# Optimization experiments

Hardware: AMD Instinct MI355X
Metric: run time of the kernel (lower is better)

The kernel has to match this reference:

```python
import jax, jax.numpy as jnp
import numpy as np

NUM_HEADS = 16


def setup_inputs() -> dict:
    key = jax.random.key(0)
    ks = jax.random.split(key, 6)
    B, S, H = 4, 2048, 1024
    x = jax.random.normal(ks[0], (B, S, H), dtype=jnp.float32)
    mask = jax.random.randint(ks[1], (B, 1, 1, S), 0, 2, dtype=jnp.int32)
    scale = 1.0 / np.sqrt(H)
    Wq = jax.random.normal(ks[2], (H, H), dtype=jnp.float32) * scale
    Wk = jax.random.normal(ks[3], (H, H), dtype=jnp.float32) * scale
    Wv = jax.random.normal(ks[4], (H, H), dtype=jnp.float32) * scale
    Wo = jax.random.normal(ks[5], (H, H), dtype=jnp.float32) * scale
    bo = jnp.zeros((H,), dtype=jnp.float32)
    return {"x": x, "mask": mask, "Wq": Wq, "Wk": Wk, "Wv": Wv, "Wo": Wo, "bo": bo}


def reference(x, mask, Wq, Wk, Wv, Wo, bo):
    B, S, H = x.shape
    nh = NUM_HEADS
    dk = H // nh

    def split_heads(t):  # (B,S,H) -> (B,nh,S,dk)
        return t.reshape(B, S, nh, dk).transpose(0, 2, 1, 3)

    # torch Linear: y = x @ W.T (q/k/v bias-free)
    q = split_heads(x @ Wq.T)
    k = split_heads(x @ Wk.T)
    v = split_heads(x @ Wv.T)

    scores = jnp.einsum('bhqd,bhkd->bhqk', q, k) / jnp.sqrt(jnp.float32(dk))
    scores = jnp.where(mask == 0, jnp.float32(-1e9), scores)
    attn = jax.nn.softmax(scores, axis=-1)  # dropout is identity in eval mode
    out = jnp.einsum('bhqk,bhkd->bhqd', attn, v)
    out = out.transpose(0, 2, 1, 3).reshape(B, S, H)
    return out @ Wo.T + bo
```

## Files before the change

### kernel.cpp

```cpp
#include <hip/hip_runtime.h>
#include <hip/hip_bf16.h>

typedef __attribute__((ext_vector_type(8))) short sh8;
typedef __attribute__((ext_vector_type(4))) float f32x4;

#define MFMA16(a, b, c) __builtin_amdgcn_mfma_f32_16x16x32_bf16((a), (b), (c), 0, 0, 0)

__device__ __forceinline__ unsigned short f2bf(float f) {
    return (unsigned short)((__float_as_uint(f) + 0x8000u) >> 16);
}
__device__ __forceinline__ unsigned int pack2bf(float lo, float hi) {
    unsigned int ul = __float_as_uint(lo) + 0x8000u;
    unsigned int uh = __float_as_uint(hi) + 0x8000u;
    return __builtin_amdgcn_perm(uh, ul, 0x07060302u);
}
__device__ __forceinline__ float redmax_hi(float x) {
    x = fmaxf(x, __shfl_xor(x, 16, 64));
    return fmaxf(x, __shfl_xor(x, 32, 64));
}
__device__ __forceinline__ float redsum_hi(float x) {
    x += __shfl_xor(x, 16, 64);
    return x + __shfl_xor(x, 32, 64);
}
__device__ __forceinline__ void gload_lds16(const void* g, void* l) {
    __builtin_amdgcn_global_load_lds(
        (const __attribute__((address_space(1))) unsigned int*)g,
        (__attribute__((address_space(3))) unsigned int*)l, 16, 0, 0);
}

__global__ __launch_bounds__(256) void cvt_x_k(
    const float* __restrict__ src, unsigned short* __restrict__ dst, int n4)
{
    int i = blockIdx.x * 256 + threadIdx.x;
    int stride = gridDim.x * 256;
    for (; i < n4; i += stride) {
        float4 v = ((const float4*)src)[i];
        uint2 h = { pack2bf(v.x, v.y), pack2bf(v.z, v.w) };
        ((uint2*)dst)[i] = h;
    }
}
__global__ __launch_bounds__(256) void cvt_w_k(
    const float* __restrict__ Wq, const float* __restrict__ Wk,
    const float* __restrict__ Wv, const float* __restrict__ Wo,
    unsigned short* __restrict__ wbf)
{
    int i = blockIdx.x * 256 + threadIdx.x;
    int seg = i >> 18;
    int off = i & 0x3FFFF;
    const float* s = (seg < 2) ? ((seg == 0) ? Wq : Wk) : ((seg == 2) ? Wv : Wo);
    float4 v = ((const float4*)s)[off];
    uint2 h = { pack2bf(v.x, v.y), pack2bf(v.z, v.w) };
    ((uint2*)wbf)[i] = h;
}

__global__ __launch_bounds__(64) void compact_k(
    const int* __restrict__ mask, int* __restrict__ idx, int* __restrict__ cnt)
{
    const int b = blockIdx.x, l = threadIdx.x;
    const int* mb = mask + b * 2048;
    int base = 0;
    for (int i = 0; i < 32; ++i) {
        int m = mb[i * 64 + l];
        unsigned long long bal = __ballot(m != 0);
        int pre = __popcll(bal & ((1ull << l) - 1ull));
        if (m) idx[b * 2048 + base + pre] = i * 64 + l;
        base += (int)__popcll(bal);
    }
    if (base == 0) {
        for (int i = l; i < 2048; i += 64) idx[b * 2048 + i] = i;
        base = 2048;
    }
    if (l == 0) cnt[b] = base;
}

__global__ __launch_bounds__(256) void kvgather_k(
    const unsigned short* __restrict__ qkv, const int* __restrict__ idx,
    const int* __restrict__ cnt, unsigned short* __restrict__ Kck, int b0)
{
    const int b = blockIdx.z;
    const int t = blockIdx.y;
    const int z = blockIdx.x;
    const int nc = cnt[b0 + b];
    if (t * 64 >= ((nc + 63) & ~63)) return;
    const int* idxb = idx + (size_t)(b0 + b) * 2048;
    const int tid = threadIdx.x;
    unsigned short* dst_b = Kck + (size_t)b * 2048 * 1024;
#pragma unroll
    for (int p = 0; p < 4; ++p) {
        int i = p * 256 + tid;
        int r = t * 64 + z * 8 + (i >> 7);
        int c = i & 127;
        int src = idxb[min(r, nc - 1)];
        uint4 v = *(const uint4*)&qkv[((size_t)b * 2048 + src) * 3072 + 1024 + c * 8];
        *(uint4*)&dst_b[(size_t)r * 1024 + c * 8] = v;
    }
}

__global__ __launch_bounds__(256) void vtrans_k(
    const unsigned short* __restrict__ qkv, const int* __restrict__ idx,
    const int* __restrict__ cnt, unsigned short* __restrict__ Vtg, int b0)
{
    __shared__ unsigned short Ls[128][72];
    const int kb = blockIdx.x;
    const int h  = blockIdx.y;
    const int b  = blockIdx.z;
    const int nc = cnt[b0 + b];
    if (kb * 128 >= ((nc + 63) & ~63)) return;
    const int* idxb = idx + (size_t)(b0 + b) * 2048;
    const int tid = threadIdx.x;
#pragma unroll
    for (int p = 0; p < 4; ++p) {
        int i = p * 256 + tid;
        int r = i >> 3, c = i & 7;
        int src = idxb[min(kb * 128 + r, nc - 1)];
        uint4 v = *(const uint4*)&qkv[((size_t)b * 2048 + src) * 3072 + 2048 + h * 64 + c * 8];
        *(uint4*)&Ls[r][c * 8] = v;
    }
    __syncthreads();
    unsigned short* dst = Vtg + ((size_t)b * 16 + h) * 64 * 2048;
#pragma unroll
    for (int p = 0; p < 4; ++p) {
        int i = p * 256 + tid;
        int d = i >> 4, kc = i & 15;
        unsigned int wv[4];
#pragma unroll
        for (int j = 0; j < 4; ++j) {
            unsigned int lo = Ls[kc * 8 + 2 * j][d];
            unsigned int hv = Ls[kc * 8 + 2 * j + 1][d];
            wv[j] = lo | (hv << 16);
        }
        *(uint4*)&dst[(size_t)d * 2048 + kb * 128 + kc * 8] = *(uint4*)wv;
    }
}

__global__ __launch_bounds__(256) void gemm_qkv_k(
    const unsigned short* __restrict__ xbf,
    const unsigned short* __restrict__ wbf,
    unsigned short* __restrict__ qkv)
{
    __shared__ unsigned short As[128][32];
    __shared__ unsigned short Bs[128][32];
    const int tid = threadIdx.x;
    const int l = tid & 63, w = tid >> 6;
    const int wr = w >> 1, wc = w & 1;
    const long row0 = (long)blockIdx.y * 128;
    const int col0 = blockIdx.x * 128;

    f32x4 acc[4][4] = {};
    const int fr = l & 15, hi = l >> 4;

    const int sr = tid >> 2;
    const int sc = (tid & 3) * 8;
    const unsigned short* ga = &xbf[(row0 + sr) * 1024 + sc];
    const unsigned short* gb = &wbf[(long)(col0 + sr) * 1024 + sc];
    unsigned short* la = &As[w * 16][0];
    unsigned short* lb = &Bs[w * 16][0];

    for (int k0 = 0; k0 < 1024; k0 += 32) {
        __syncthreads();
        gload_lds16(ga + k0, la);
        gload_lds16(ga + 64 * 1024 + k0, la + 64 * 32);
        gload_lds16(gb + k0, lb);
        gload_lds16(gb + 64 * 1024 + k0, lb + 64 * 32);
        __syncthreads();

        sh8 af[4], bf[4];
#pragma unroll
        for (int i = 0; i < 4; ++i) {
            af[i] = *(const sh8*)&As[wr * 64 + i * 16 + fr][hi * 8];
            bf[i] = *(const sh8*)&Bs[wc * 64 + i * 16 + fr][hi * 8];
        }
#pragma unroll
        for (int i = 0; i < 4; ++i)
#pragma unroll
            for (int j = 0; j < 4; ++j)
                acc[i][j] = MFMA16(af[i], bf[j], acc[i][j]);
    }

    const float scale = (col0 < 1024) ? 0.1803368801f : 1.0f;
    const int rg = hi * 4, cg = l & 15;
#pragma unroll
    for (int i = 0; i < 4; ++i)
#pragma unroll
        for (int j = 0; j < 4; ++j) {
            long gr = row0 + wr * 64 + i * 16 + rg;
            int gc = col0 + wc * 64 + j * 16 + cg;
#pragma unroll
            for (int r = 0; r < 4; ++r)
                qkv[(gr + r) * 3072 + gc] = f2bf(acc[i][j][r] * scale);
        }
}

__global__ __launch_bounds__(256) void attn_k(
    const unsigned short* __restrict__ qkv, const unsigned short* __restrict__ Kck,
    const unsigned short* __restrict__ Vtg, const int* __restrict__ cnt,
    unsigned short* __restrict__ ao, int b0)
{
    __shared__ unsigned short Kl[64][64];
    __shared__ unsigned short Vt[64][64];
    __shared__ float biasf[64];
    __shared__ unsigned short Pl[4][16][72];

    const int tid = threadIdx.x;
    const int l = tid & 63, w = tid >> 6;
    const int fr = l & 15, hi = l >> 4;

    int nwg = gridDim.x;
    int wgid = ((nwg & 7) == 0) ? ((blockIdx.x & 7) * (nwg >> 3) + (blockIdx.x >> 3))
                                : blockIdx.x;
    const int qb = wgid & 31;
    const int h  = (wgid >> 5) & 15;
    const int b  = wgid >> 9;
    const int q0 = qb * 64;
    const long base = (long)b * 2048;

    const int nc = cnt[b0 + b];
    const int nt = (nc + 63) >> 6;

    sh8 qf0, qf1;
    {
        const unsigned short* qp = &qkv[(base + q0 + w * 16 + fr) * 3072 + h * 64 + hi * 8];
        qf0 = *(const sh8*)qp;
        qf1 = *(const sh8*)(qp + 32);
    }

    f32x4 acc[4] = {};
    float mrow = -1e30f;
    float lrow = 0.f;

    const long TSK = 131072;
    const char* kck_b = (const char*)Kck + (size_t)b * 2048 * 2048;

    const int l8 = l >> 3, c8 = l & 7;
    const char* ksrc = kck_b + (size_t)(w * 16 + l8) * 2048 + h * 128 + ((c8 ^ l8) * 16);
    unsigned short* kdst0 = &Kl[w * 16][0];
    unsigned short* kdst1 = &Kl[w * 16 + 8][0];

    const char* vtg_h = (const char*)Vtg + ((size_t)b * 16 + h) * 64 * 4096;
    const int d0 = w * 16 + l8, d1 = d0 + 8;
    const int fd0 = (d0 & 7) ^ (d0 >> 3), fd1 = (d1 & 7) ^ (d1 >> 3);
    const char* vsrc0 = vtg_h + (size_t)d0 * 4096 + ((c8 ^ fd0) * 16);
    const char* vsrc1 = vtg_h + (size_t)d1 * 4096 + ((c8 ^ fd1) * 16);
    unsigned short* vdst0 = &Vt[w * 16][0];
    unsigned short* vdst1 = &Vt[w * 16 + 8][0];

    if (tid < 64) biasf[tid] = ((nt - 1) * 64 + tid < nc) ? 0.0f : -1e9f;

    for (int t = 0; t < nt; ++t) {
        __syncthreads();
        gload_lds16(ksrc, kdst0);
        gload_lds16(ksrc + 8 * 2048, kdst1);
        ksrc += TSK;
        gload_lds16(vsrc0, vdst0);
        gload_lds16(vsrc1, vdst1);
        vsrc0 += 128; vsrc1 += 128;
        __syncthreads();

        sh8 kf[4][2];
#pragma unroll
        for (int tt = 0; tt < 4; ++tt) {
            const unsigned short* kp = &Kl[tt * 16 + fr][0];
#pragma unroll
            for (int c = 0; c < 2; ++c)
                kf[tt][c] = *(const sh8*)&kp[((4 * c + hi) ^ (fr & 7)) * 8];
        }

        f32x4 s[4] = {};
        __builtin_amdgcn_s_setprio(1);
#pragma unroll
        for (int tt = 0; tt < 4; ++tt) {
            s[tt] = MFMA16(kf[tt][0], qf0, s[tt]);
            s[tt] = MFMA16(kf[tt][1], qf1, s[tt]);
        }
        __builtin_amdgcn_s_setprio(0);

        if (t == nt - 1) {
#pragma unroll
            for (int tt = 0; tt < 4; ++tt)
                s[tt] += *(const f32x4*)&biasf[tt * 16 + 4 * hi];
        }

        float pm = s[0][0];
#pragma unroll
        for (int tt = 0; tt < 4; ++tt)
#pragma unroll
            for (int r = 0; r < 4; ++r) pm = fmaxf(pm, s[tt][r]);
        pm = redmax_hi(pm);

        if (!__all(pm <= mrow)) {
            float mn = fmaxf(mrow, pm);
            float scl = __builtin_amdgcn_exp2f(mrow - mn);
            lrow *= scl;
#pragma unroll
            for (int df = 0; df < 4; ++df) acc[df] *= scl;
            mrow = mn;
        }

        float ps = 0.f;
#pragma unroll
        for (int tt = 0; tt < 4; ++tt)
#pragma unroll
            for (int r = 0; r < 4; ++r) {
                float p = __builtin_amdgcn_exp2f(s[tt][r] - mrow);
                s[tt][r] = p;
                ps += p;
            }
        lrow += redsum_hi(ps);

#pragma unroll
        for (int tt = 0; tt < 4; ++tt) {
            uint2 pw = { pack2bf(s[tt][0], s[tt][1]), pack2bf(s[tt][2], s[tt][3]) };
            *(uint2*)&Pl[w][fr][tt * 16 + hi * 4] = pw;
        }

#pragma unroll
        for (int c = 0; c < 2; ++c) {
            sh8 pa = *(const sh8*)&Pl[w][fr][c * 32 + hi * 8];
            __builtin_amdgcn_s_setprio(1);
#pragma unroll
            for (int df = 0; df < 4; ++df) {
                int d = df * 16 + fr;
                int fd = (d & 7) ^ (d >> 3);
                sh8 vfr = *(const sh8*)&Vt[d][((4 * c + hi) ^ fd) * 8];
                acc[df] = MFMA16(vfr, pa, acc[df]);
            }
            __builtin_amdgcn_s_setprio(0);
        }
    }

    {
        float inv = 1.0f / lrow;
        long qr = base + q0 + w * 16 + fr;
        unsigned short* op = &ao[qr * 1024 + h * 64];
#pragma unroll
        for (int df = 0; df < 4; ++df) {
            f32x4 o = acc[df];
            uint2 ow = { pack2bf(o[0] * inv, o[1] * inv), pack2bf(o[2] * inv, o[3] * inv) };
            *(uint2*)&op[df * 16 + hi * 4] = ow;
        }
    }
}

__global__ __launch_bounds__(256) void gemm_out_k(
    const unsigned short* __restrict__ ao, const unsigned short* __restrict__ wob,
    const float* __restrict__ bo, float* __restrict__ out)
{
    __shared__ unsigned short As[128][32];
    __shared__ unsigned short Bs[128][32];
    const int tid = threadIdx.x;
    const int l = tid & 63, w = tid >> 6;
    const int wr = w >> 1, wc = w & 1;
    const long row0 = (long)blockIdx.y * 128;
    const int col0 = blockIdx.x * 128;

    f32x4 acc[4][4] = {};
    const int fr = l & 15, hi = l >> 4;

    const int sr = tid >> 2;
    const int sc = (tid & 3) * 8;
    const unsigned short* ga = &ao[(row0 + sr) * 1024 + sc];
    const unsigned short* gb = &wob[(long)(col0 + sr) * 1024 + sc];
    unsigned short* la = &As[w * 16][0];
    unsigned short* lb = &Bs[w * 16][0];

    for (int k0 = 0; k0 < 1024; k0 += 32) {
        __syncthreads();
        gload_lds16(ga + k0, la);
        gload_lds16(ga + 64 * 1024 + k0, la + 64 * 32);
        gload_lds16(gb + k0, lb);
        gload_lds16(gb + 64 * 1024 + k0, lb + 64 * 32);
        __syncthreads();

        sh8 af[4], bf[4];
#pragma unroll
        for (int i = 0; i < 4; ++i) {
            af[i] = *(const sh8*)&As[wr * 64 + i * 16 + fr][hi * 8];
            bf[i] = *(const sh8*)&Bs[wc * 64 + i * 16 + fr][hi * 8];
        }
#pragma unroll
        for (int i = 0; i < 4; ++i)
#pragma unroll
            for (int j = 0; j < 4; ++j)
                acc[i][j] = MFMA16(af[i], bf[j], acc[i][j]);
    }

    const int rg = hi * 4, cg = l & 15;
#pragma unroll
    for (int i = 0; i < 4; ++i)
#pragma unroll
        for (int j = 0; j < 4; ++j) {
            long gr = row0 + wr * 64 + i * 16 + rg;
            int gc = col0 + wc * 64 + j * 16 + cg;
            float bb = bo[gc];
#pragma unroll
            for (int r = 0; r < 4; ++r)
                out[(gr + r) * 1024 + gc] = acc[i][j][r] + bb;
        }
}

extern "C" void kernel_launch(void* const* d_in, const int* in_sizes, int n_in,
                              void* d_out, int out_size, void* d_ws, size_t ws_size,
                              hipStream_t stream) {
    const float* x    = (const float*)d_in[0];
    const int*   mask = (const int*)d_in[1];
    const float* Wq   = (const float*)d_in[2];
    const float* Wk   = (const float*)d_in[3];
    const float* Wv   = (const float*)d_in[4];
    const float* Wo   = (const float*)d_in[5];
    const float* bo   = (const float*)d_in[6];
    float* out = (float*)d_out;

    const size_t wbf_bytes = (size_t)4096 * 1024 * 2;
    const size_t idx_bytes = (size_t)4 * 2048 * 4 + 64;
    const size_t xbf_per_b = (size_t)2048 * 1024 * 2;
    const size_t qkv_per_b = (size_t)2048 * 3072 * 2;
    const size_t ao_per_b  = (size_t)2048 * 1024 * 2;
    const size_t kck_per_b = (size_t)2048 * 1024 * 2;
    const size_t vt_per_b  = (size_t)16 * 64 * 2048 * 2;
    const size_t per_b = xbf_per_b + qkv_per_b + ao_per_b + kck_per_b + vt_per_b;

    size_t fixed = wbf_bytes + idx_bytes;
    size_t avail = (ws_size > fixed) ? (ws_size - fixed) : 0;
    int bchunk = (avail >= per_b) ? (int)(avail / per_b) : 1;
    if (bchunk > 4) bchunk = 4;

    char* p = (char*)d_ws;
    unsigned short* wbf = (unsigned short*)p;            p += wbf_bytes;
    int* idxp = (int*)p;                                 p += (size_t)4 * 2048 * 4;
    int* cntp = (int*)p;                                 p += 64;
    unsigned short* xbf = (unsigned short*)p;            p += (size_t)bchunk * xbf_per_b;
    unsigned short* qkv = (unsigned short*)p;            p += (size_t)bchunk * qkv_per_b;
    unsigned short* ao  = (unsigned short*)p;            p += (size_t)bchunk * ao_per_b;
    unsigned short* Kck = (unsigned short*)p;            p += (size_t)bchunk * kck_per_b;
    unsigned short* Vtg = (unsigned short*)p;

    cvt_w_k<<<4096, 256, 0, stream>>>(Wq, Wk, Wv, Wo, wbf);
    compact_k<<<4, 64, 0, stream>>>(mask, idxp, cntp);

    for (int b0 = 0; b0 < 4; b0 += bchunk) {
        int bc = (4 - b0 < bchunk) ? (4 - b0) : bchunk;
        cvt_x_k<<<2048, 256, 0, stream>>>(
            x + (size_t)b0 * 2048 * 1024, xbf, bc * 524288);
        gemm_qkv_k<<<dim3(24, bc * 16), 256, 0, stream>>>(xbf, wbf, qkv);
        kvgather_k<<<dim3(8, 32, bc), 256, 0, stream>>>(qkv, idxp, cntp, Kck, b0);
        vtrans_k<<<dim3(16, 16, bc), 256, 0, stream>>>(qkv, idxp, cntp, Vtg, b0);
        attn_k<<<dim3(512 * bc), 256, 0, stream>>>(qkv, Kck, Vtg, cntp, ao, b0);
        gemm_out_k<<<dim3(8, bc * 16), 256, 0, stream>>>(
            ao, wbf + (size_t)3072 * 1024, bo, out + (size_t)b0 * 2048 * 1024);
    }
}
```

Baseline: 213.5 us.

## Process two query groups per wave in attention and compute row sums via MFMA

Each attention workgroup now handles 128 query rows instead of 64, with each wave owning two 16-row groups. The K and V tiles loaded into LDS are therefore reused across twice as many queries, and the grid is halved. The softmax row-sum is now accumulated with an extra MFMA against a ones vector instead of a shuffle reduction, so it is computed from the bf16-rounded probabilities. The cost is higher register pressure and fewer workgroups, which may reduce occupancy and parallelism.

```diff
diff --git a/kernel.cpp b/kernel.cpp
--- a/kernel.cpp
+++ b/kernel.cpp
@@ -17,10 +17,6 @@
 __device__ __forceinline__ float redmax_hi(float x) {
     x = fmaxf(x, __shfl_xor(x, 16, 64));
     return fmaxf(x, __shfl_xor(x, 32, 64));
-}
-__device__ __forceinline__ float redsum_hi(float x) {
-    x += __shfl_xor(x, 16, 64);
-    return x + __shfl_xor(x, 32, 64);
 }
 __device__ __forceinline__ void gload_lds16(const void* g, void* l) {
     __builtin_amdgcn_global_load_lds(
@@ -199,7 +195,7 @@
     __shared__ unsigned short Kl[64][64];
     __shared__ unsigned short Vt[64][64];
     __shared__ float biasf[64];
-    __shared__ unsigned short Pl[4][16][72];
+    __shared__ unsigned short Pl[4][2][16][72];
 
     const int tid = threadIdx.x;
     const int l = tid & 63, w = tid >> 6;
@@ -208,25 +204,30 @@
     int nwg = gridDim.x;
     int wgid = ((nwg & 7) == 0) ? ((blockIdx.x & 7) * (nwg >> 3) + (blockIdx.x >> 3))
                                 : blockIdx.x;
-    const int qb = wgid & 31;
-    const int h  = (wgid >> 5) & 15;
-    const int b  = wgid >> 9;
-    const int q0 = qb * 64;
+    const int qb = wgid & 15;
+    const int h  = (wgid >> 4) & 15;
+    const int b  = wgid >> 8;
+    const int q0 = qb * 128;
     const long base = (long)b * 2048;
 
     const int nc = cnt[b0 + b];
     const int nt = (nc + 63) >> 6;
 
-    sh8 qf0, qf1;
-    {
-        const unsigned short* qp = &qkv[(base + q0 + w * 16 + fr) * 3072 + h * 64 + hi * 8];
-        qf0 = *(const sh8*)qp;
-        qf1 = *(const sh8*)(qp + 32);
-    }
-
-    f32x4 acc[4] = {};
-    float mrow = -1e30f;
-    float lrow = 0.f;
+    sh8 qf[2][2];
+#pragma unroll
+    for (int g = 0; g < 2; ++g) {
+        const unsigned short* qp = &qkv[(base + q0 + w * 32 + g * 16 + fr) * 3072 + h * 64 + hi * 8];
+        qf[g][0] = *(const sh8*)qp;
+        qf[g][1] = *(const sh8*)(qp + 32);
+    }
+
+    sh8 ones8;
+#pragma unroll
+    for (int i = 0; i < 8; ++i) ones8[i] = (short)0x3F80;
+
+    f32x4 acc[2][4] = {};
+    f32x4 accs[2] = {};
+    float mrow[2] = { -1e30f, -1e30f };
 
     const long TSK = 131072;
     const char* kck_b = (const char*)Kck + (size_t)b * 2048 * 2048;
@@ -265,76 +266,76 @@
                 kf[tt][c] = *(const sh8*)&kp[((4 * c + hi) ^ (fr & 7)) * 8];
         }
 
-        f32x4 s[4] = {};
-        __builtin_amdgcn_s_setprio(1);
-#pragma unroll
-        for (int tt = 0; tt < 4; ++tt) {
-            s[tt] = MFMA16(kf[tt][0], qf0, s[tt]);
-            s[tt] = MFMA16(kf[tt][1], qf1, s[tt]);
-        }
-        __builtin_amdgcn_s_setprio(0);
-
-        if (t == nt - 1) {
+#pragma unroll
+        for (int g = 0; g < 2; ++g) {
+            f32x4 s[4] = {};
+            __builtin_amdgcn_s_setprio(1);
+#pragma unroll
+            for (int tt = 0; tt < 4; ++tt) {
+                s[tt] = MFMA16(kf[tt][0], qf[g][0], s[tt]);
+                s[tt] = MFMA16(kf[tt][1], qf[g][1], s[tt]);
+            }
+            __builtin_amdgcn_s_setprio(0);
+
+            if (t == nt - 1) {
+#pragma unroll
+                for (int tt = 0; tt < 4; ++tt)
+                    s[tt] += *(const f32x4*)&biasf[tt * 16 + 4 * hi];
+            }
+
+            float pm = s[0][0];
 #pragma unroll
             for (int tt = 0; tt < 4; ++tt)
-                s[tt] += *(const f32x4*)&biasf[tt * 16 + 4 * hi];
-        }
-
-        float pm = s[0][0];
-#pragma unroll
-        for (int tt = 0; tt < 4; ++tt)
-#pragma unroll
-            for (int r = 0; r < 4; ++r) pm = fmaxf(pm, s[tt][r]);
-        pm = redmax_hi(pm);
-
-        if (!__all(pm <= mrow)) {
-            float mn = fmaxf(mrow, pm);
-            float scl = __builtin_amdgcn_exp2f(mrow - mn);
-            lrow *= scl;
-#pragma unroll
-            for (int df = 0; df < 4; ++df) acc[df] *= scl;
-            mrow = mn;
-        }
-
-        float ps = 0.f;
-#pragma unroll
-        for (int tt = 0; tt < 4; ++tt)
-#pragma unroll
-            for (int r = 0; r < 4; ++r) {
-                float p = __builtin_amdgcn_exp2f(s[tt][r] - mrow);
-                s[tt][r] = p;
-                ps += p;
+#pragma unroll
+                for (int r = 0; r < 4; ++r) pm = fmaxf(pm, s[tt][r]);
+            pm = redmax_hi(pm);
+
+            if (!__all(pm <= mrow[g])) {
+                float mn = fmaxf(mrow[g], pm);
+                float scl = __builtin_amdgcn_exp2f(mrow[g] - mn);
+                accs[g] *= scl;
+#pragma unroll
+                for (int df = 0; df < 4; ++df) acc[g][df] *= scl;
+                mrow[g] = mn;
             }
-        lrow += redsum_hi(ps);
-
-#pragma unroll
-        for (int tt = 0; tt < 4; ++tt) {
-            uint2 pw = { pack2bf(s[tt][0], s[tt][1]), pack2bf(s[tt][2], s[tt][3]) };
-            *(uint2*)&Pl[w][fr][tt * 16 + hi * 4] = pw;
+
+#pragma unroll
+            for (int tt = 0; tt < 4; ++tt) {
+#pragma unroll
+                for (int r = 0; r < 4; ++r)
+                    s[tt][r] = __builtin_amdgcn_exp2f(s[tt][r] - mrow[g]);
+                uint2 pw = { pack2bf(s[tt][0], s[tt][1]), pack2bf(s[tt][2], s[tt][3]) };
+                *(uint2*)&Pl[w][g][fr][tt * 16 + hi * 4] = pw;
+            }
         }
 
 #pragma unroll
         for (int c = 0; c < 2; ++c) {
-            sh8 pa = *(const sh8*)&Pl[w][fr][c * 32 + hi * 8];
+            sh8 pa0 = *(const sh8*)&Pl[w][0][fr][c * 32 + hi * 8];
+            sh8 pa1 = *(const sh8*)&Pl[w][1][fr][c * 32 + hi * 8];
             __builtin_amdgcn_s_setprio(1);
+            accs[0] = MFMA16(ones8, pa0, accs[0]);
+            accs[1] = MFMA16(ones8, pa1, accs[1]);
 #pragma unroll
             for (int df = 0; df < 4; ++df) {
                 int d = df * 16 + fr;
                 int fd = (d & 7) ^ (d >> 3);
                 sh8 vfr = *(const sh8*)&Vt[d][((4 * c + hi) ^ fd) * 8];
-                acc[df] = MFMA16(vfr, pa, acc[df]);
+                acc[0][df] = MFMA16(vfr, pa0, acc[0][df]);
+                acc[1][df] = MFMA16(vfr, pa1, acc[1][df]);
             }
             __builtin_amdgcn_s_setprio(0);
         }
     }
 
-    {
-        float inv = 1.0f / lrow;
-        long qr = base + q0 + w * 16 + fr;
+#pragma unroll
+    for (int g = 0; g < 2; ++g) {
+        float inv = 1.0f / accs[g][0];
+        long qr = base + q0 + w * 32 + g * 16 + fr;
         unsigned short* op = &ao[qr * 1024 + h * 64];
 #pragma unroll
         for (int df = 0; df < 4; ++df) {
-            f32x4 o = acc[df];
+            f32x4 o = acc[g][df];
             uint2 ow = { pack2bf(o[0] * inv, o[1] * inv), pack2bf(o[2] * inv, o[3] * inv) };
             *(uint2*)&op[df * 16 + hi * 4] = ow;
         }
@@ -444,7 +445,7 @@
         gemm_qkv_k<<<dim3(24, bc * 16), 256, 0, stream>>>(xbf, wbf, qkv);
         kvgather_k<<<dim3(8, 32, bc), 256, 0, stream>>>(qkv, idxp, cntp, Kck, b0);
         vtrans_k<<<dim3(16, 16, bc), 256, 0, stream>>>(qkv, idxp, cntp, Vtg, b0);
-        attn_k<<<dim3(512 * bc), 256, 0, stream>>>(qkv, Kck, Vtg, cntp, ao, b0);
+        attn_k<<<dim3(256 * bc), 256, 0, stream>>>(qkv, Kck, Vtg, cntp, ao, b0);
         gemm_out_k<<<dim3(8, bc * 16), 256, 0, stream>>>(
             ao, wbf + (size_t)3072 * 1024, bo, out + (size_t)b0 * 2048 * 1024);
     }
```

After: 216.0 us. Within noise of the previous version (+1.2%).

## Double-buffer K/V tiles in LDS and prefetch next tile during compute

Applied to the files above, without the earlier changes.

The attention kernel now keeps two LDS buffers each for K and V. The first tile is loaded before the loop, and each iteration issues the async global-to-LDS loads for the next tile before computing on the current one. This drops one barrier per iteration and aims to hide global load latency behind the QK and PV MFMAs. The cost is about 16KB more LDS per block, which may lower occupancy. If the compiler inserts a full vmcnt wait before the LDS reads, the loads may not overlap with compute at all.

```diff
diff --git a/kernel.cpp b/kernel.cpp
--- a/kernel.cpp
+++ b/kernel.cpp
@@ -196,8 +196,8 @@
     const unsigned short* __restrict__ Vtg, const int* __restrict__ cnt,
     unsigned short* __restrict__ ao, int b0)
 {
-    __shared__ unsigned short Kl[64][64];
-    __shared__ unsigned short Vt[64][64];
+    __shared__ unsigned short Kl[2][64][64];
+    __shared__ unsigned short Vt[2][64][64];
     __shared__ float biasf[64];
     __shared__ unsigned short Pl[4][16][72];
 
@@ -233,33 +233,39 @@
 
     const int l8 = l >> 3, c8 = l & 7;
     const char* ksrc = kck_b + (size_t)(w * 16 + l8) * 2048 + h * 128 + ((c8 ^ l8) * 16);
-    unsigned short* kdst0 = &Kl[w * 16][0];
-    unsigned short* kdst1 = &Kl[w * 16 + 8][0];
 
     const char* vtg_h = (const char*)Vtg + ((size_t)b * 16 + h) * 64 * 4096;
     const int d0 = w * 16 + l8, d1 = d0 + 8;
     const int fd0 = (d0 & 7) ^ (d0 >> 3), fd1 = (d1 & 7) ^ (d1 >> 3);
     const char* vsrc0 = vtg_h + (size_t)d0 * 4096 + ((c8 ^ fd0) * 16);
     const char* vsrc1 = vtg_h + (size_t)d1 * 4096 + ((c8 ^ fd1) * 16);
-    unsigned short* vdst0 = &Vt[w * 16][0];
-    unsigned short* vdst1 = &Vt[w * 16 + 8][0];
 
     if (tid < 64) biasf[tid] = ((nt - 1) * 64 + tid < nc) ? 0.0f : -1e9f;
+
+    gload_lds16(ksrc, &Kl[0][w * 16][0]);
+    gload_lds16(ksrc + 8 * 2048, &Kl[0][w * 16 + 8][0]);
+    ksrc += TSK;
+    gload_lds16(vsrc0, &Vt[0][w * 16][0]);
+    gload_lds16(vsrc1, &Vt[0][w * 16 + 8][0]);
+    vsrc0 += 128; vsrc1 += 128;
 
     for (int t = 0; t < nt; ++t) {
         __syncthreads();
-        gload_lds16(ksrc, kdst0);
-        gload_lds16(ksrc + 8 * 2048, kdst1);
-        ksrc += TSK;
-        gload_lds16(vsrc0, vdst0);
-        gload_lds16(vsrc1, vdst1);
-        vsrc0 += 128; vsrc1 += 128;
-        __syncthreads();
+        const int cur = t & 1;
+        if (t + 1 < nt) {
+            const int nxt = cur ^ 1;
+            gload_lds16(ksrc, &Kl[nxt][w * 16][0]);
+            gload_lds16(ksrc + 8 * 2048, &Kl[nxt][w * 16 + 8][0]);
+            ksrc += TSK;
+            gload_lds16(vsrc0, &Vt[nxt][w * 16][0]);
+            gload_lds16(vsrc1, &Vt[nxt][w * 16 + 8][0]);
+            vsrc0 += 128; vsrc1 += 128;
+        }
 
         sh8 kf[4][2];
 #pragma unroll
         for (int tt = 0; tt < 4; ++tt) {
-            const unsigned short* kp = &Kl[tt * 16 + fr][0];
+            const unsigned short* kp = &Kl[cur][tt * 16 + fr][0];
 #pragma unroll
             for (int c = 0; c < 2; ++c)
                 kf[tt][c] = *(const sh8*)&kp[((4 * c + hi) ^ (fr & 7)) * 8];
@@ -321,7 +327,7 @@
             for (int df = 0; df < 4; ++df) {
                 int d = df * 16 + fr;
                 int fd = (d & 7) ^ (d >> 3);
-                sh8 vfr = *(const sh8*)&Vt[d][((4 * c + hi) ^ fd) * 8];
+                sh8 vfr = *(const sh8*)&Vt[cur][d][((4 * c + hi) ^ fd) * 8];
                 acc[df] = MFMA16(vfr, pa, acc[df]);
             }
             __builtin_amdgcn_s_setprio(0);
```

Result: slower. 220.9 us (+3.5%).

## Register-prefetch next K/V tile instead of direct global-to-LDS loads

Applied to the files above, without the earlier changes.

Replaces the direct global-to-LDS async loads of each K and V tile with a register-staged software pipeline. The next tile's global loads are issued into registers right after the current tile is written to LDS, so their latency overlaps with the QK^T/softmax/PV compute. Swizzling moves from the global source address to the LDS destination address. This costs extra VGPRs and explicit LDS store instructions, and may lower occupancy.

```diff
diff --git a/kernel.cpp b/kernel.cpp
--- a/kernel.cpp
+++ b/kernel.cpp
@@ -230,31 +230,42 @@
 
     const long TSK = 131072;
     const char* kck_b = (const char*)Kck + (size_t)b * 2048 * 2048;
+    const char* vtg_h = (const char*)Vtg + ((size_t)b * 16 + h) * 64 * 4096;
 
     const int l8 = l >> 3, c8 = l & 7;
-    const char* ksrc = kck_b + (size_t)(w * 16 + l8) * 2048 + h * 128 + ((c8 ^ l8) * 16);
-    unsigned short* kdst0 = &Kl[w * 16][0];
-    unsigned short* kdst1 = &Kl[w * 16 + 8][0];
-
-    const char* vtg_h = (const char*)Vtg + ((size_t)b * 16 + h) * 64 * 4096;
+    const char* ksrc = kck_b + (size_t)(w * 16 + l8) * 2048 + h * 128 + c8 * 16;
     const int d0 = w * 16 + l8, d1 = d0 + 8;
+    const char* vsrc0 = vtg_h + (size_t)d0 * 4096 + c8 * 16;
+    const char* vsrc1 = vtg_h + (size_t)d1 * 4096 + c8 * 16;
+    unsigned short* kd0 = &Kl[w * 16 + l8][(c8 ^ l8) * 8];
+    unsigned short* kd1 = &Kl[w * 16 + 8 + l8][(c8 ^ l8) * 8];
     const int fd0 = (d0 & 7) ^ (d0 >> 3), fd1 = (d1 & 7) ^ (d1 >> 3);
-    const char* vsrc0 = vtg_h + (size_t)d0 * 4096 + ((c8 ^ fd0) * 16);
-    const char* vsrc1 = vtg_h + (size_t)d1 * 4096 + ((c8 ^ fd1) * 16);
-    unsigned short* vdst0 = &Vt[w * 16][0];
-    unsigned short* vdst1 = &Vt[w * 16 + 8][0];
+    unsigned short* vd0 = &Vt[d0][(c8 ^ fd0) * 8];
+    unsigned short* vd1 = &Vt[d1][(c8 ^ fd1) * 8];
 
     if (tid < 64) biasf[tid] = ((nt - 1) * 64 + tid < nc) ? 0.0f : -1e9f;
 
+    uint4 k0r = *(const uint4*)ksrc;
+    uint4 k1r = *(const uint4*)(ksrc + 8 * 2048);
+    uint4 v0r = *(const uint4*)vsrc0;
+    uint4 v1r = *(const uint4*)vsrc1;
+    ksrc += TSK; vsrc0 += 128; vsrc1 += 128;
+
     for (int t = 0; t < nt; ++t) {
         __syncthreads();
-        gload_lds16(ksrc, kdst0);
-        gload_lds16(ksrc + 8 * 2048, kdst1);
-        ksrc += TSK;
-        gload_lds16(vsrc0, vdst0);
-        gload_lds16(vsrc1, vdst1);
-        vsrc0 += 128; vsrc1 += 128;
-        __syncthreads();
+        *(uint4*)kd0 = k0r;
+        *(uint4*)kd1 = k1r;
+        *(uint4*)vd0 = v0r;
+        *(uint4*)vd1 = v1r;
+        __syncthreads();
+
+        if (t + 1 < nt) {
+            k0r = *(const uint4*)ksrc;
+            k1r = *(const uint4*)(ksrc + 8 * 2048);
+            v0r = *(const uint4*)vsrc0;
+            v1r = *(const uint4*)vsrc1;
+            ksrc += TSK; vsrc0 += 128; vsrc1 += 128;
+        }
 
         sh8 kf[4][2];
 #pragma unroll
```

New measurement: 216.3 us. No clear change (+1.3%).
